# Performance work log

Hardware: AMD Instinct MI355X
Metric: run time of the kernel (lower is better)

## Reference

```python
import jax, jax.numpy as jnp
import numpy as np
import math

INPUT_SIZE = 128
HIDDEN_SIZE = 64
MEM_DIM = 64
B, S = 8, 2048


def _xavier(key, shape):
    fan_in, fan_out = shape[0], shape[1]
    a = math.sqrt(6.0 / (fan_in + fan_out))
    return jax.random.uniform(key, shape, jnp.float32, minval=-a, maxval=a)


def setup_inputs() -> dict:
    key = jax.random.key(0)
    ks = jax.random.split(key, 8)
    x = jax.random.normal(ks[0], (B, S, INPUT_SIZE), jnp.float32)
    return {
        "x": x,
        "c_prev": jnp.zeros((MEM_DIM, MEM_DIM), jnp.float32),
        "n_prev": jnp.zeros((MEM_DIM, 1), jnp.float32),
        "w_q": _xavier(ks[1], (INPUT_SIZE, HIDDEN_SIZE)),
        "b_q": jnp.zeros((HIDDEN_SIZE,), jnp.float32),
        "w_k": _xavier(ks[2], (INPUT_SIZE, MEM_DIM)),
        "b_k": jnp.zeros((MEM_DIM,), jnp.float32),
        "w_v": _xavier(ks[3], (INPUT_SIZE, MEM_DIM)),
        "b_v": jnp.zeros((MEM_DIM,), jnp.float32),
        "w_i": _xavier(ks[4], (INPUT_SIZE, 1)),
        "b_i": jnp.zeros((1,), jnp.float32),
        "w_f": _xavier(ks[5], (INPUT_SIZE, 1)),
        "b_f": jnp.zeros((1,), jnp.float32),
        "w_o": _xavier(ks[6], (INPUT_SIZE, HIDDEN_SIZE)),
        "b_o": jnp.zeros((HIDDEN_SIZE,), jnp.float32),
    }


def reference(x, c_prev, n_prev, w_q, b_q, w_k, b_k, w_v, b_v,
              w_i, b_i, w_f, b_f, w_o, b_o):
    b, s, d = x.shape
    mem_dim = w_k.shape[1]
    xf = x.reshape(b * s, d)  # [T, D], T = B*S

    q_t = xf @ w_q + b_q                                   # [T, H]
    k_t = (xf @ w_k + b_k) * (1.0 / math.sqrt(mem_dim))    # [T, M]
    v_t = xf @ w_v + b_v                                   # [T, M]
    i_t = jnp.exp(xf @ w_i + b_i)                          # [T, 1]
    f_t = jax.nn.sigmoid(xf @ w_f + b_f)                   # [T, 1]

    # Faithful to source: c_prev / n_prev are NEVER updated in the loop,
    # so every step mixes the same initial state -> fully parallel.
    # c_t[t] = f[t] * c_prev + i[t] * outer(v[t], k[t])
    c_t = (f_t[:, :, None] * c_prev[None]
           + i_t[:, :, None] * v_t[:, :, None] * k_t[:, None, :])  # [T, M, M]
    # n_t[t] = f[t] * n_prev + i[t] * k[t][:, None]
    n_t = f_t[:, :, None] * n_prev[None] + i_t[:, :, None] * k_t[:, :, None]  # [T, M, 1]

    c_t = c_t.reshape(b, s, mem_dim, mem_dim)
    n_t = n_t.reshape(b, s, mem_dim, 1)
    qv = q_t.reshape(b, s, mem_dim)  # requires hidden_size == mem_dim

    nq = jnp.einsum("bsm,bsm->bs", n_t[..., 0], qv)
    max_nqt = jnp.maximum(jnp.abs(nq), 1.0)                # [B, S]
    h_tilde = jnp.einsum("bsmk,bsk->bsm", c_t, qv) / max_nqt[..., None]

    o_t = jax.nn.sigmoid(xf @ w_o + b_o).reshape(b, s, -1)
    h_t = o_t * h_tilde                                    # [B, S, H]
    return (h_t, c_t, n_t)
```

## Files before the change

kernel.cpp:

```cpp
#include <hip/hip_runtime.h>
#include <cstdint>

#define NTOK 16384

typedef float f4 __attribute__((ext_vector_type(4)));

__device__ __forceinline__ float readlane_f(float v, int lane) {
  return __int_as_float(__builtin_amdgcn_readlane(__float_as_int(v), lane));
}

__device__ __forceinline__ float wave_sum64(float v) {
  #pragma unroll
  for (int s = 1; s < 64; s <<= 1) v += __shfl_xor(v, s, 64);
  return v;
}

__device__ __forceinline__ float half_sum32(float v) {
  #pragma unroll
  for (int s = 1; s < 32; s <<= 1) v += __shfl_xor(v, s, 64);
  return v;
}

__device__ __forceinline__ float elemf(f4 v, int e) {
  return e == 0 ? v.x : e == 1 ? v.y : e == 2 ? v.z : v.w;
}

__global__ void __launch_bounds__(512, 2)
fused_kernel(const float* __restrict__ x,
             const float* __restrict__ c_prev,
             const float* __restrict__ n_prev,
             const float* __restrict__ w_q, const float* __restrict__ b_q,
             const float* __restrict__ w_k, const float* __restrict__ b_k,
             const float* __restrict__ w_v, const float* __restrict__ b_v,
             const float* __restrict__ w_i, const float* __restrict__ b_i,
             const float* __restrict__ w_f, const float* __restrict__ b_f,
             const float* __restrict__ w_o, const float* __restrict__ b_o,
             float* __restrict__ h_out,
             float* __restrict__ c_out,
             float* __restrict__ n_out)
{
  __shared__ uint32_t wlds[4][64][64];
  __shared__ float    cp[64][68];
  const int tid = threadIdx.x;

  {
    const float* Ws[4] = {w_q, w_k, w_v, w_o};
    #pragma unroll
    for (int m = 0; m < 4; ++m) {
      const float* W = Ws[m];
      #pragma unroll
      for (int it = 0; it < 8; ++it) {
        int idx = it * 512 + tid;
        int dp  = idx >> 6;
        int j   = idx & 63;
        uint32_t ua = __float_as_uint(W[(2 * dp)     * 64 + j]);
        uint32_t ub = __float_as_uint(W[(2 * dp + 1) * 64 + j]);
        ua = (ua + 0x7FFFu + ((ua >> 16) & 1u)) >> 16;
        ub = (ub + 0x7FFFu + ((ub >> 16) & 1u)) >> 16;
        wlds[m][j][dp ^ ((j & 7) << 2)] = (ua & 0xFFFFu) | (ub << 16);
      }
    }
  }
  for (int idx = tid; idx < 4096; idx += 512)
    cp[idx >> 6][idx & 63] = c_prev[idx];
  __syncthreads();

  const int lane = tid & 63;
  const int wid  = tid >> 6;
  const int t0   = blockIdx.x * 64 + wid * 8;

  const f4* xp = (const f4*)(x + (size_t)t0 * 128);
  f4 xc[4];
  xc[0] = xp[lane];
  xc[1] = xp[64 + lane];
  xc[2] = xp[128 + lane];
  xc[3] = xp[192 + lane];

  const float bq = b_q[lane], bk = b_k[lane], bv = b_v[lane], bo = b_o[lane];
  float accq[8], acck[8], accv[8], acco[8];
  #pragma unroll
  for (int tt = 0; tt < 8; ++tt) { accq[tt] = bq; acck[tt] = bk; accv[tt] = bv; acco[tt] = bo; }

  #pragma unroll 2
  for (int dp4 = 0; dp4 < 16; ++dp4) {
    const int off = (dp4 * 4) ^ ((lane & 7) << 2);
    const uint4 uq = *(const uint4*)&wlds[0][lane][off];
    const uint4 uk = *(const uint4*)&wlds[1][lane][off];
    const uint4 uv = *(const uint4*)&wlds[2][lane][off];
    const uint4 uo = *(const uint4*)&wlds[3][lane][off];
    #pragma unroll
    for (int e = 0; e < 4; ++e) {
      const uint32_t cq = (&uq.x)[e], ck = (&uk.x)[e];
      const uint32_t cv = (&uv.x)[e], co = (&uo.x)[e];
      const float wq0 = __uint_as_float(cq << 16), wq1 = __uint_as_float(cq & 0xFFFF0000u);
      const float wk0 = __uint_as_float(ck << 16), wk1 = __uint_as_float(ck & 0xFFFF0000u);
      const float wv0 = __uint_as_float(cv << 16), wv1 = __uint_as_float(cv & 0xFFFF0000u);
      const float wo0 = __uint_as_float(co << 16), wo1 = __uint_as_float(co & 0xFFFF0000u);
      const int lsub = 2 * dp4 + (e >> 1);
      #pragma unroll
      for (int tt = 0; tt < 8; ++tt) {
        const int lidx = ((tt & 1) << 5) + lsub;
        const float xa = readlane_f(elemf(xc[tt >> 1], (2 * e) & 3), lidx);
        const float xb = readlane_f(elemf(xc[tt >> 1], (2 * e + 1) & 3), lidx);
        accq[tt] = fmaf(wq0, xa, accq[tt]); accq[tt] = fmaf(wq1, xb, accq[tt]);
        acck[tt] = fmaf(wk0, xa, acck[tt]); acck[tt] = fmaf(wk1, xb, acck[tt]);
        accv[tt] = fmaf(wv0, xa, accv[tt]); accv[tt] = fmaf(wv1, xb, accv[tt]);
        acco[tt] = fmaf(wo0, xa, acco[tt]); acco[tt] = fmaf(wo1, xb, acco[tt]);
      }
    }
  }

  float itv[8], ftv[8];
  {
    const int dbase = (lane & 31) << 2;
    const f4 wi4 = *(const f4*)&w_i[dbase];
    const f4 wf4 = *(const f4*)&w_f[dbase];
    const float sbi = b_i[0], sbf = b_f[0];
    #pragma unroll
    for (int c = 0; c < 4; ++c) {
      float pi = xc[c].x * wi4.x + xc[c].y * wi4.y + xc[c].z * wi4.z + xc[c].w * wi4.w;
      float pf = xc[c].x * wf4.x + xc[c].y * wf4.y + xc[c].z * wf4.z + xc[c].w * wf4.w;
      pi = half_sum32(pi);
      pf = half_sum32(pf);
      itv[2 * c]     = __expf(readlane_f(pi, 0)  + sbi);
      itv[2 * c + 1] = __expf(readlane_f(pi, 32) + sbi);
      ftv[2 * c]     = 1.0f / (1.0f + __expf(-(readlane_f(pf, 0)  + sbf)));
      ftv[2 * c + 1] = 1.0f / (1.0f + __expf(-(readlane_f(pf, 32) + sbf)));
    }
  }

  const float npv = n_prev[lane];
  const int m = lane & 15;
  #pragma unroll
  for (int tt = 0; tt < 8; ++tt) {
    const size_t t = (size_t)(t0 + tt);
    const float q   = accq[tt];
    const float k   = acck[tt] * 0.125f;
    const float v   = accv[tt];
    const float o   = 1.0f / (1.0f + __expf(-acco[tt]));
    const float it_ = itv[tt];
    const float ft_ = ftv[tt];

    const float n_val = fmaf(ft_, npv, it_ * k);
    n_out[t * 64 + lane] = n_val;

    const float nq = wave_sum64(n_val * q);
    const float kq = wave_sum64(k * q);

    float c0 = 0.f, c1 = 0.f, c2 = 0.f, c3 = 0.f;
    #pragma unroll
    for (int j = 0; j < 16; ++j) {
      const f4 r4 = *(const f4*)&cp[lane][4 * j];
      c0 = fmaf(r4.x, readlane_f(q, 4 * j),     c0);
      c1 = fmaf(r4.y, readlane_f(q, 4 * j + 1), c1);
      c2 = fmaf(r4.z, readlane_f(q, 4 * j + 2), c2);
      c3 = fmaf(r4.w, readlane_f(q, 4 * j + 3), c3);
    }
    const float cpq = (c0 + c1) + (c2 + c3);

    const float inv  = 1.0f / fmaxf(fabsf(nq), 1.0f);
    const float htil = fmaf(ft_, cpq, it_ * v * kq) * inv;
    h_out[t * 64 + lane] = o * htil;

    const float iv = it_ * v;
    const float k40 = __shfl(k, 4 * m, 64);
    const float k41 = __shfl(k, 4 * m + 1, 64);
    const float k42 = __shfl(k, 4 * m + 2, 64);
    const float k43 = __shfl(k, 4 * m + 3, 64);
    f4* ct = (f4*)(c_out + t * 4096);
    #pragma unroll
    for (int s = 0; s < 16; ++s) {
      const int row = 4 * s + (lane >> 4);
      const float ivr = __shfl(iv, row, 64);
      const f4 c4 = *(const f4*)&cp[row][4 * m];
      f4 val;
      val.x = fmaf(ft_, c4.x, ivr * k40);
      val.y = fmaf(ft_, c4.y, ivr * k41);
      val.z = fmaf(ft_, c4.z, ivr * k42);
      val.w = fmaf(ft_, c4.w, ivr * k43);
      ct[s * 64 + lane] = val;
    }
  }
}

extern "C" void kernel_launch(void* const* d_in, const int* in_sizes, int n_in,
                              void* d_out, int out_size, void* d_ws, size_t ws_size,
                              hipStream_t stream) {
  const float* x      = (const float*)d_in[0];
  const float* c_prev = (const float*)d_in[1];
  const float* n_prev = (const float*)d_in[2];
  const float* w_q = (const float*)d_in[3];
  const float* b_q = (const float*)d_in[4];
  const float* w_k = (const float*)d_in[5];
  const float* b_k = (const float*)d_in[6];
  const float* w_v = (const float*)d_in[7];
  const float* b_v = (const float*)d_in[8];
  const float* w_i = (const float*)d_in[9];
  const float* b_i = (const float*)d_in[10];
  const float* w_f = (const float*)d_in[11];
  const float* b_f = (const float*)d_in[12];
  const float* w_o = (const float*)d_in[13];
  const float* b_o = (const float*)d_in[14];

  float* h_out = (float*)d_out;
  float* c_out = h_out + 1048576;
  float* n_out = c_out + 67108864;

  fused_kernel<<<256, 512, 0, stream>>>(x, c_prev, n_prev,
                                        w_q, b_q, w_k, b_k, w_v, b_v,
                                        w_i, b_i, w_f, b_f, w_o, b_o,
                                        h_out, c_out, n_out);
}
```

Measured before the change: 60.50 us.

## Interleave projection and c_t store phases in groups of two tokens

Instead of computing all eight token projections first and then writing outputs, each wave now loops over four groups of two tokens, computing projections and immediately emitting n, h and the large c_t stores. The next x chunk is prefetched during each group. The aim is to spread the heavy c_out store traffic across the kernel so compute from one group overlaps stores from the previous one, and to cut accumulator register pressure. The cost is that LDS weights are re-read four times per wave and the loop is not unrolled.

```diff
diff --git a/kernel.cpp b/kernel.cpp
--- a/kernel.cpp
+++ b/kernel.cpp
@@ -69,117 +69,118 @@
   const int wid  = tid >> 6;
   const int t0   = blockIdx.x * 64 + wid * 8;
 
+  const float bq = b_q[lane], bk = b_k[lane], bv = b_v[lane], bo = b_o[lane];
+  const float npv = n_prev[lane];
+  const int   m   = lane & 15;
+  const int   dbase = (lane & 31) << 2;
+  const f4 wi4 = *(const f4*)&w_i[dbase];
+  const f4 wf4 = *(const f4*)&w_f[dbase];
+  const float sbi = b_i[0], sbf = b_f[0];
+
   const f4* xp = (const f4*)(x + (size_t)t0 * 128);
-  f4 xc[4];
-  xc[0] = xp[lane];
-  xc[1] = xp[64 + lane];
-  xc[2] = xp[128 + lane];
-  xc[3] = xp[192 + lane];
-
-  const float bq = b_q[lane], bk = b_k[lane], bv = b_v[lane], bo = b_o[lane];
-  float accq[8], acck[8], accv[8], acco[8];
-  #pragma unroll
-  for (int tt = 0; tt < 8; ++tt) { accq[tt] = bq; acck[tt] = bk; accv[tt] = bv; acco[tt] = bo; }
-
-  #pragma unroll 2
-  for (int dp4 = 0; dp4 < 16; ++dp4) {
-    const int off = (dp4 * 4) ^ ((lane & 7) << 2);
-    const uint4 uq = *(const uint4*)&wlds[0][lane][off];
-    const uint4 uk = *(const uint4*)&wlds[1][lane][off];
-    const uint4 uv = *(const uint4*)&wlds[2][lane][off];
-    const uint4 uo = *(const uint4*)&wlds[3][lane][off];
-    #pragma unroll
-    for (int e = 0; e < 4; ++e) {
-      const uint32_t cq = (&uq.x)[e], ck = (&uk.x)[e];
-      const uint32_t cv = (&uv.x)[e], co = (&uo.x)[e];
-      const float wq0 = __uint_as_float(cq << 16), wq1 = __uint_as_float(cq & 0xFFFF0000u);
-      const float wk0 = __uint_as_float(ck << 16), wk1 = __uint_as_float(ck & 0xFFFF0000u);
-      const float wv0 = __uint_as_float(cv << 16), wv1 = __uint_as_float(cv & 0xFFFF0000u);
-      const float wo0 = __uint_as_float(co << 16), wo1 = __uint_as_float(co & 0xFFFF0000u);
-      const int lsub = 2 * dp4 + (e >> 1);
-      #pragma unroll
-      for (int tt = 0; tt < 8; ++tt) {
-        const int lidx = ((tt & 1) << 5) + lsub;
-        const float xa = readlane_f(elemf(xc[tt >> 1], (2 * e) & 3), lidx);
-        const float xb = readlane_f(elemf(xc[tt >> 1], (2 * e + 1) & 3), lidx);
-        accq[tt] = fmaf(wq0, xa, accq[tt]); accq[tt] = fmaf(wq1, xb, accq[tt]);
-        acck[tt] = fmaf(wk0, xa, acck[tt]); acck[tt] = fmaf(wk1, xb, acck[tt]);
-        accv[tt] = fmaf(wv0, xa, accv[tt]); accv[tt] = fmaf(wv1, xb, accv[tt]);
-        acco[tt] = fmaf(wo0, xa, acco[tt]); acco[tt] = fmaf(wo1, xb, acco[tt]);
-      }
-    }
-  }
-
-  float itv[8], ftv[8];
-  {
-    const int dbase = (lane & 31) << 2;
-    const f4 wi4 = *(const f4*)&w_i[dbase];
-    const f4 wf4 = *(const f4*)&w_f[dbase];
-    const float sbi = b_i[0], sbf = b_f[0];
-    #pragma unroll
-    for (int c = 0; c < 4; ++c) {
-      float pi = xc[c].x * wi4.x + xc[c].y * wi4.y + xc[c].z * wi4.z + xc[c].w * wi4.w;
-      float pf = xc[c].x * wf4.x + xc[c].y * wf4.y + xc[c].z * wf4.z + xc[c].w * wf4.w;
+  f4 xg = xp[lane];
+
+  #pragma unroll 1
+  for (int g = 0; g < 4; ++g) {
+    const f4 xnext = xp[((g + 1) & 3) * 64 + lane];
+
+    float aq[2], ak[2], av[2], ao[2];
+    aq[0] = aq[1] = bq; ak[0] = ak[1] = bk;
+    av[0] = av[1] = bv; ao[0] = ao[1] = bo;
+
+    #pragma unroll 2
+    for (int dp4 = 0; dp4 < 16; ++dp4) {
+      const int off = (dp4 * 4) ^ ((lane & 7) << 2);
+      const uint4 uq = *(const uint4*)&wlds[0][lane][off];
+      const uint4 uk = *(const uint4*)&wlds[1][lane][off];
+      const uint4 uv = *(const uint4*)&wlds[2][lane][off];
+      const uint4 uo = *(const uint4*)&wlds[3][lane][off];
+      #pragma unroll
+      for (int e = 0; e < 4; ++e) {
+        const uint32_t cq = (&uq.x)[e], ck = (&uk.x)[e];
+        const uint32_t cv = (&uv.x)[e], co = (&uo.x)[e];
+        const float wq0 = __uint_as_float(cq << 16), wq1 = __uint_as_float(cq & 0xFFFF0000u);
+        const float wk0 = __uint_as_float(ck << 16), wk1 = __uint_as_float(ck & 0xFFFF0000u);
+        const float wv0 = __uint_as_float(cv << 16), wv1 = __uint_as_float(cv & 0xFFFF0000u);
+        const float wo0 = __uint_as_float(co << 16), wo1 = __uint_as_float(co & 0xFFFF0000u);
+        const int lsub = 2 * dp4 + (e >> 1);
+        #pragma unroll
+        for (int tt = 0; tt < 2; ++tt) {
+          const int lidx = (tt << 5) + lsub;
+          const float xa = readlane_f(elemf(xg, (2 * e) & 3), lidx);
+          const float xb = readlane_f(elemf(xg, (2 * e + 1) & 3), lidx);
+          aq[tt] = fmaf(wq0, xa, aq[tt]); aq[tt] = fmaf(wq1, xb, aq[tt]);
+          ak[tt] = fmaf(wk0, xa, ak[tt]); ak[tt] = fmaf(wk1, xb, ak[tt]);
+          av[tt] = fmaf(wv0, xa, av[tt]); av[tt] = fmaf(wv1, xb, av[tt]);
+          ao[tt] = fmaf(wo0, xa, ao[tt]); ao[tt] = fmaf(wo1, xb, ao[tt]);
+        }
+      }
+    }
+
+    float it01[2], ft01[2];
+    {
+      float pi = xg.x * wi4.x + xg.y * wi4.y + xg.z * wi4.z + xg.w * wi4.w;
+      float pf = xg.x * wf4.x + xg.y * wf4.y + xg.z * wf4.z + xg.w * wf4.w;
       pi = half_sum32(pi);
       pf = half_sum32(pf);
-      itv[2 * c]     = __expf(readlane_f(pi, 0)  + sbi);
-      itv[2 * c + 1] = __expf(readlane_f(pi, 32) + sbi);
-      ftv[2 * c]     = 1.0f / (1.0f + __expf(-(readlane_f(pf, 0)  + sbf)));
-      ftv[2 * c + 1] = 1.0f / (1.0f + __expf(-(readlane_f(pf, 32) + sbf)));
-    }
-  }
-
-  const float npv = n_prev[lane];
-  const int m = lane & 15;
-  #pragma unroll
-  for (int tt = 0; tt < 8; ++tt) {
-    const size_t t = (size_t)(t0 + tt);
-    const float q   = accq[tt];
-    const float k   = acck[tt] * 0.125f;
-    const float v   = accv[tt];
-    const float o   = 1.0f / (1.0f + __expf(-acco[tt]));
-    const float it_ = itv[tt];
-    const float ft_ = ftv[tt];
-
-    const float n_val = fmaf(ft_, npv, it_ * k);
-    n_out[t * 64 + lane] = n_val;
-
-    const float nq = wave_sum64(n_val * q);
-    const float kq = wave_sum64(k * q);
-
-    float c0 = 0.f, c1 = 0.f, c2 = 0.f, c3 = 0.f;
+      it01[0] = __expf(readlane_f(pi, 0)  + sbi);
+      it01[1] = __expf(readlane_f(pi, 32) + sbi);
+      ft01[0] = 1.0f / (1.0f + __expf(-(readlane_f(pf, 0)  + sbf)));
+      ft01[1] = 1.0f / (1.0f + __expf(-(readlane_f(pf, 32) + sbf)));
+    }
+
     #pragma unroll
-    for (int j = 0; j < 16; ++j) {
-      const f4 r4 = *(const f4*)&cp[lane][4 * j];
-      c0 = fmaf(r4.x, readlane_f(q, 4 * j),     c0);
-      c1 = fmaf(r4.y, readlane_f(q, 4 * j + 1), c1);
-      c2 = fmaf(r4.z, readlane_f(q, 4 * j + 2), c2);
-      c3 = fmaf(r4.w, readlane_f(q, 4 * j + 3), c3);
-    }
-    const float cpq = (c0 + c1) + (c2 + c3);
-
-    const float inv  = 1.0f / fmaxf(fabsf(nq), 1.0f);
-    const float htil = fmaf(ft_, cpq, it_ * v * kq) * inv;
-    h_out[t * 64 + lane] = o * htil;
-
-    const float iv = it_ * v;
-    const float k40 = __shfl(k, 4 * m, 64);
-    const float k41 = __shfl(k, 4 * m + 1, 64);
-    const float k42 = __shfl(k, 4 * m + 2, 64);
-    const float k43 = __shfl(k, 4 * m + 3, 64);
-    f4* ct = (f4*)(c_out + t * 4096);
-    #pragma unroll
-    for (int s = 0; s < 16; ++s) {
-      const int row = 4 * s + (lane >> 4);
-      const float ivr = __shfl(iv, row, 64);
-      const f4 c4 = *(const f4*)&cp[row][4 * m];
-      f4 val;
-      val.x = fmaf(ft_, c4.x, ivr * k40);
-      val.y = fmaf(ft_, c4.y, ivr * k41);
-      val.z = fmaf(ft_, c4.z, ivr * k42);
-      val.w = fmaf(ft_, c4.w, ivr * k43);
-      ct[s * 64 + lane] = val;
-    }
+    for (int tt = 0; tt < 2; ++tt) {
+      const size_t t = (size_t)(t0 + 2 * g + tt);
+      const float q   = aq[tt];
+      const float k   = ak[tt] * 0.125f;
+      const float v   = av[tt];
+      const float o   = 1.0f / (1.0f + __expf(-ao[tt]));
+      const float it_ = it01[tt];
+      const float ft_ = ft01[tt];
+
+      const float n_val = fmaf(ft_, npv, it_ * k);
+      n_out[t * 64 + lane] = n_val;
+
+      const float nq = wave_sum64(n_val * q);
+      const float kq = wave_sum64(k * q);
+
+      float c0 = 0.f, c1 = 0.f, c2 = 0.f, c3 = 0.f;
+      #pragma unroll
+      for (int j = 0; j < 16; ++j) {
+        const f4 r4 = *(const f4*)&cp[lane][4 * j];
+        c0 = fmaf(r4.x, readlane_f(q, 4 * j),     c0);
+        c1 = fmaf(r4.y, readlane_f(q, 4 * j + 1), c1);
+        c2 = fmaf(r4.z, readlane_f(q, 4 * j + 2), c2);
+        c3 = fmaf(r4.w, readlane_f(q, 4 * j + 3), c3);
+      }
+      const float cpq = (c0 + c1) + (c2 + c3);
+
+      const float inv  = 1.0f / fmaxf(fabsf(nq), 1.0f);
+      const float htil = fmaf(ft_, cpq, it_ * v * kq) * inv;
+      h_out[t * 64 + lane] = o * htil;
+
+      const float iv = it_ * v;
+      const float k40 = __shfl(k, 4 * m, 64);
+      const float k41 = __shfl(k, 4 * m + 1, 64);
+      const float k42 = __shfl(k, 4 * m + 2, 64);
+      const float k43 = __shfl(k, 4 * m + 3, 64);
+      f4* ct = (f4*)(c_out + t * 4096);
+      #pragma unroll
+      for (int s = 0; s < 16; ++s) {
+        const int row = 4 * s + (lane >> 4);
+        const float ivr = __shfl(iv, row, 64);
+        const f4 c4 = *(const f4*)&cp[row][4 * m];
+        f4 val;
+        val.x = fmaf(ft_, c4.x, ivr * k40);
+        val.y = fmaf(ft_, c4.y, ivr * k41);
+        val.z = fmaf(ft_, c4.z, ivr * k42);
+        val.w = fmaf(ft_, c4.w, ivr * k43);
+        ct[s * 64 + lane] = val;
+      }
+    }
+
+    xg = xnext;
   }
 }
 
```

New measurement: 62.67 us. 1.04x slower.

## Compute q/k/v/o projections with bf16 MFMA and stage results through LDS

Applied to the files above, without the earlier changes.

Replaces the scalar FMA projection loop, which broadcast x values lane by lane via readlane, with bf16 16x16x32 MFMA instructions. Each wave computes a 16-token by 128-feature tile, and the results go through shared memory so every wave can read its own 8 tokens' q/k/v/o. The per-token epilogue loop is no longer unrolled. This adds two barriers and an LDS round-trip and also converts x to bf16. The kernel is likely dominated by the 256MB c_out write, so the projection speedup may matter little.

```diff
diff --git a/kernel.cpp b/kernel.cpp
--- a/kernel.cpp
+++ b/kernel.cpp
@@ -4,6 +4,8 @@
 #define NTOK 16384
 
 typedef float f4 __attribute__((ext_vector_type(4)));
+typedef __attribute__((ext_vector_type(4))) float f32x4;
+typedef __attribute__((ext_vector_type(8))) short bf16x8;
 
 __device__ __forceinline__ float readlane_f(float v, int lane) {
   return __int_as_float(__builtin_amdgcn_readlane(__float_as_int(v), lane));
@@ -21,8 +23,9 @@
   return v;
 }
 
-__device__ __forceinline__ float elemf(f4 v, int e) {
-  return e == 0 ? v.x : e == 1 ? v.y : e == 2 ? v.z : v.w;
+__device__ __forceinline__ uint32_t rne_bf16(float f) {
+  uint32_t u = __float_as_uint(f);
+  return (u + 0x7FFFu + ((u >> 16) & 1u)) >> 16;
 }
 
 __global__ void __launch_bounds__(512, 2)
@@ -39,76 +42,90 @@
              float* __restrict__ c_out,
              float* __restrict__ n_out)
 {
-  __shared__ uint32_t wlds[4][64][64];
+  __shared__ uint32_t smem[16384];
   __shared__ float    cp[64][68];
-  const int tid = threadIdx.x;
-
-  {
-    const float* Ws[4] = {w_q, w_k, w_v, w_o};
-    #pragma unroll
-    for (int m = 0; m < 4; ++m) {
-      const float* W = Ws[m];
-      #pragma unroll
-      for (int it = 0; it < 8; ++it) {
-        int idx = it * 512 + tid;
-        int dp  = idx >> 6;
-        int j   = idx & 63;
-        uint32_t ua = __float_as_uint(W[(2 * dp)     * 64 + j]);
-        uint32_t ub = __float_as_uint(W[(2 * dp + 1) * 64 + j]);
-        ua = (ua + 0x7FFFu + ((ua >> 16) & 1u)) >> 16;
-        ub = (ub + 0x7FFFu + ((ub >> 16) & 1u)) >> 16;
-        wlds[m][j][dp ^ ((j & 7) << 2)] = (ua & 0xFFFFu) | (ub << 16);
-      }
+  const int tid  = threadIdx.x;
+  const int lane = tid & 63;
+  const int wid  = tid >> 6;
+  const int T0   = blockIdx.x * 64;
+
+  {
+    const int n   = tid & 255;
+    const int col = n & 63;
+    const float* W = (n < 128) ? ((n < 64) ? w_q : w_k)
+                               : ((n < 192) ? w_v : w_o);
+    const int kph = tid >> 8;
+    #pragma unroll
+    for (int it = 0; it < 32; ++it) {
+      const int kp = it * 2 + kph;
+      const float a = W[(2 * kp)     * 64 + col];
+      const float b = W[(2 * kp + 1) * 64 + col];
+      const uint32_t pk = rne_bf16(a) | (rne_bf16(b) << 16);
+      const int unit = (n << 4) + ((kp >> 2) ^ (n & 15));
+      smem[(unit << 2) + (kp & 3)] = pk;
     }
   }
   for (int idx = tid; idx < 4096; idx += 512)
     cp[idx >> 6][idx & 63] = c_prev[idx];
-  __syncthreads();
-
-  const int lane = tid & 63;
-  const int wid  = tid >> 6;
-  const int t0   = blockIdx.x * 64 + wid * 8;
-
-  const f4* xp = (const f4*)(x + (size_t)t0 * 128);
+
+  const f4* xp = (const f4*)(x + (size_t)(T0 + wid * 8) * 128);
   f4 xc[4];
   xc[0] = xp[lane];
   xc[1] = xp[64 + lane];
   xc[2] = xp[128 + lane];
   xc[3] = xp[192 + lane];
 
-  const float bq = b_q[lane], bk = b_k[lane], bv = b_v[lane], bo = b_o[lane];
-  float accq[8], acck[8], accv[8], acco[8];
+  __syncthreads();
+
+  const int mt  = wid & 3;
+  const int ntg = (wid >> 2) * 8;
+  bf16x8 afrag[4];
+  {
+    const float* xr = x + (size_t)(T0 + mt * 16 + (lane & 15)) * 128
+                        + ((lane >> 4) * 8);
+    #pragma unroll
+    for (int ks = 0; ks < 4; ++ks) {
+      const f4 lo = *(const f4*)(xr + ks * 32);
+      const f4 hi = *(const f4*)(xr + ks * 32 + 4);
+      union { uint32_t u[4]; bf16x8 v; } cv;
+      cv.u[0] = rne_bf16(lo.x) | (rne_bf16(lo.y) << 16);
+      cv.u[1] = rne_bf16(lo.z) | (rne_bf16(lo.w) << 16);
+      cv.u[2] = rne_bf16(hi.x) | (rne_bf16(hi.y) << 16);
+      cv.u[3] = rne_bf16(hi.z) | (rne_bf16(hi.w) << 16);
+      afrag[ks] = cv.v;
+    }
+  }
+  f32x4 acc[8];
   #pragma unroll
-  for (int tt = 0; tt < 8; ++tt) { accq[tt] = bq; acck[tt] = bk; accv[tt] = bv; acco[tt] = bo; }
-
-  #pragma unroll 2
-  for (int dp4 = 0; dp4 < 16; ++dp4) {
-    const int off = (dp4 * 4) ^ ((lane & 7) << 2);
-    const uint4 uq = *(const uint4*)&wlds[0][lane][off];
-    const uint4 uk = *(const uint4*)&wlds[1][lane][off];
-    const uint4 uv = *(const uint4*)&wlds[2][lane][off];
-    const uint4 uo = *(const uint4*)&wlds[3][lane][off];
-    #pragma unroll
-    for (int e = 0; e < 4; ++e) {
-      const uint32_t cq = (&uq.x)[e], ck = (&uk.x)[e];
-      const uint32_t cv = (&uv.x)[e], co = (&uo.x)[e];
-      const float wq0 = __uint_as_float(cq << 16), wq1 = __uint_as_float(cq & 0xFFFF0000u);
-      const float wk0 = __uint_as_float(ck << 16), wk1 = __uint_as_float(ck & 0xFFFF0000u);
-      const float wv0 = __uint_as_float(cv << 16), wv1 = __uint_as_float(cv & 0xFFFF0000u);
-      const float wo0 = __uint_as_float(co << 16), wo1 = __uint_as_float(co & 0xFFFF0000u);
-      const int lsub = 2 * dp4 + (e >> 1);
+  for (int j = 0; j < 8; ++j) acc[j] = (f32x4){0.f, 0.f, 0.f, 0.f};
+  {
+    const int bsub = lane & 15, bh = lane >> 4;
+    #pragma unroll
+    for (int nti = 0; nti < 8; ++nti) {
+      const int n = (ntg + nti) * 16 + bsub;
       #pragma unroll
-      for (int tt = 0; tt < 8; ++tt) {
-        const int lidx = ((tt & 1) << 5) + lsub;
-        const float xa = readlane_f(elemf(xc[tt >> 1], (2 * e) & 3), lidx);
-        const float xb = readlane_f(elemf(xc[tt >> 1], (2 * e + 1) & 3), lidx);
-        accq[tt] = fmaf(wq0, xa, accq[tt]); accq[tt] = fmaf(wq1, xb, accq[tt]);
-        acck[tt] = fmaf(wk0, xa, acck[tt]); acck[tt] = fmaf(wk1, xb, acck[tt]);
-        accv[tt] = fmaf(wv0, xa, accv[tt]); accv[tt] = fmaf(wv1, xb, accv[tt]);
-        acco[tt] = fmaf(wo0, xa, acco[tt]); acco[tt] = fmaf(wo1, xb, acco[tt]);
+      for (int ks = 0; ks < 4; ++ks) {
+        const int unit = (n << 4) + ((ks * 4 + bh) ^ (n & 15));
+        const bf16x8 bfrag = *(const bf16x8*)&smem[unit << 2];
+        acc[nti] = __builtin_amdgcn_mfma_f32_16x16x32_bf16(afrag[ks], bfrag,
+                                                           acc[nti], 0, 0, 0);
       }
     }
   }
+  __syncthreads();
+  {
+    float* y = (float*)smem;
+    const int trow = mt * 16 + (lane >> 4) * 4;
+    const int fcol = lane & 15;
+    #pragma unroll
+    for (int nti = 0; nti < 8; ++nti) {
+      const int f = (ntg + nti) * 16 + fcol;
+      #pragma unroll
+      for (int r = 0; r < 4; ++r)
+        y[(trow + r) * 256 + f] = acc[nti][r];
+    }
+  }
+  __syncthreads();
 
   float itv[8], ftv[8];
   {
@@ -129,15 +146,19 @@
     }
   }
 
+  const float bq = b_q[lane], bk = b_k[lane], bv = b_v[lane], bo = b_o[lane];
   const float npv = n_prev[lane];
-  const int m = lane & 15;
-  #pragma unroll
+  const int   m   = lane & 15;
+  const float* y  = (const float*)smem;
+
+  #pragma unroll 1
   for (int tt = 0; tt < 8; ++tt) {
-    const size_t t = (size_t)(t0 + tt);
-    const float q   = accq[tt];
-    const float k   = acck[tt] * 0.125f;
-    const float v   = accv[tt];
-    const float o   = 1.0f / (1.0f + __expf(-acco[tt]));
+    const int    tl = wid * 8 + tt;
+    const size_t t  = (size_t)(T0 + tl);
+    const float q   = y[tl * 256 + lane] + bq;
+    const float k   = (y[tl * 256 + 64 + lane] + bk) * 0.125f;
+    const float v   = y[tl * 256 + 128 + lane] + bv;
+    const float o   = 1.0f / (1.0f + __expf(-(y[tl * 256 + 192 + lane] + bo)));
     const float it_ = itv[tt];
     const float ft_ = ftv[tt];
 
```

Measured after the change: 55.66 us. -8.0%, faster.
